# Kernel tuning notes

Measured on AMD Instinct MI355X. Metric: run time of the kernel, lower is better.

Reference implementation:

```python
import jax, jax.numpy as jnp
import numpy as np
import math

B, N, D, H, K = 32, 512, 768, 12, 8  # batch, patches, hidden_dim, heads, n_topic_groups
HD = D // H


def setup_inputs() -> dict:
    key = jax.random.key(0)
    ks = jax.random.split(key, 12)
    hidden_states = jax.random.normal(ks[0], (B, N, D), jnp.float32)
    # group ids in 1..K, every group present (required by original sorted-dict indexing)
    tid = jax.random.permutation(ks[1], (jnp.arange(B, dtype=jnp.int64) % K) + 1)
    s = 1.0 / math.sqrt(D)
    def lin(k):
        kw, kb = jax.random.split(k)
        return (jax.random.normal(kw, (D, D), jnp.float32) * s,
                jax.random.normal(kb, (D,), jnp.float32) * s)
    Wq, bq = lin(ks[2])
    Wk, bk = lin(ks[3])
    Wv, bv = lin(ks[4])
    Wo, bo = lin(ks[5])
    Wc, bc = lin(ks[6])  # Conv1d(D, D, kernel_size=1) == pointwise linear
    return dict(hidden_states=hidden_states, tid=tid, Wq=Wq, bq=bq, Wk=Wk, bk=bk,
                Wv=Wv, bv=bv, Wo=Wo, bo=bo, Wc=Wc, bc=bc)


def reference(hidden_states, tid, Wq, bq, Wk, bk, Wv, bv, Wo, bo, Wc, bc):
    # --- context(): per-group context_aware + mean, scattered back ---
    # context_aware(x) = mean over group of (x + conv1x1(x)); conv is pointwise so
    # it commutes with grouping -> compute per-sample then segment-mean.
    y = hidden_states + jnp.einsum('bnd,ed->bne', hidden_states, Wc) + bc  # [B,N,D]
    seg = tid - 1  # ids are 1..K
    sums = jax.ops.segment_sum(y, seg, num_segments=K)                      # [K,N,D]
    counts = jax.ops.segment_sum(jnp.ones((B,), y.dtype), seg, num_segments=K)
    means = sums / jnp.maximum(counts, 1.0)[:, None, None]
    contexts = means[seg] + hidden_states                                   # [B,N,D]

    # --- dual-stage attention (dropout rate 0 / eval mode) ---
    def heads(x):  # [B,N,D] -> [B,H,N,HD]
        return x.reshape(B, N, H, HD).transpose(0, 2, 1, 3)

    q = heads(hidden_states @ Wq.T + bq)
    t = heads(contexts @ Wq.T + bq)  # topic_states also passes through self.query
    k = heads(hidden_states @ Wk.T + bk)
    v = heads(hidden_states @ Wv.T + bv)

    scale = 1.0 / math.sqrt(HD)
    p1 = jax.nn.softmax(jnp.einsum('bhqd,bhkd->bhqk', t, k) * scale, axis=-1)
    v_t = jnp.einsum('bhqk,bhkd->bhqd', p1, v)
    p2 = jax.nn.softmax(jnp.einsum('bhqd,bhkd->bhqk', q, t) * scale, axis=-1)
    ctx = jnp.einsum('bhqk,bhkd->bhqd', p2, v_t)

    ctx = ctx.transpose(0, 2, 1, 3).reshape(B, N, D)
    return ctx @ Wo.T + bo
```

## Files before the change

kernel.cpp:

```cpp
#include <hip/hip_runtime.h>
#include <hip/hip_bf16.h>


typedef __bf16 bf16_t;
typedef __bf16 bf16x8 __attribute__((ext_vector_type(8)));
typedef __bf16 bf16x4 __attribute__((ext_vector_type(4)));
typedef float f32x4 __attribute__((ext_vector_type(4)));

#define B_ 32
#define N_ 512
#define D_ 768
#define H_ 12
#define HD_ 64
#define K_ 8
#define ND_ (N_ * D_)

typedef __attribute__((address_space(1))) unsigned int as1_u32;
typedef __attribute__((address_space(3))) unsigned int as3_u32;

__device__ __forceinline__ void glds16(const void* g, void* l) {
  __builtin_amdgcn_global_load_lds((as1_u32*)g, (as3_u32*)l, 16, 0, 0);
}

__device__ __forceinline__ f32x4 mfma16(bf16x8 a, bf16x8 b, f32x4 c) {
  return __builtin_amdgcn_mfma_f32_16x16x32_bf16(a, b, c, 0, 0, 0);
}

__device__ __forceinline__ bf16x8 addv8(bf16x8 a, bf16x8 b) {
  bf16x8 o;
#pragma unroll
  for (int j = 0; j < 8; ++j) o[j] = (bf16_t)((float)a[j] + (float)b[j]);
  return o;
}

__device__ __forceinline__ int seg_of(const int* tid, int b) {
  const bool is64 = (tid[1] == 0);
  int v = is64 ? (int)((const long long*)tid)[b] : tid[b];
  return v - 1;
}

__global__ __launch_bounds__(256) void k_cvt_all(
    const float* __restrict__ x, const float* __restrict__ Wq,
    const float* __restrict__ Wk, const float* __restrict__ Wv,
    const float* __restrict__ Wc, const float* __restrict__ Wo,
    bf16_t* __restrict__ Xb, bf16_t* __restrict__ Wqb,
    bf16_t* __restrict__ Wkb, bf16_t* __restrict__ Wvb,
    bf16_t* __restrict__ Wcb, bf16_t* __restrict__ Wob) {
  int bid = blockIdx.x;
  const float* in;
  bf16_t* out;
  if (bid < 6144) {
    in = x; out = Xb;
  } else {
    const int wi = (bid - 6144) / 288;
    bid = (bid - 6144) % 288;
    in = wi == 0 ? Wq : wi == 1 ? Wk : wi == 2 ? Wv : wi == 3 ? Wc : Wo;
    out = wi == 0 ? Wqb : wi == 1 ? Wkb : wi == 2 ? Wvb : wi == 3 ? Wcb : Wob;
  }
  const size_t i = ((size_t)bid * 256 + threadIdx.x) * 8;
  f32x4 a = *(const f32x4*)(in + i);
  f32x4 b = *(const f32x4*)(in + i + 4);
  bf16x8 o;
#pragma unroll
  for (int j = 0; j < 4; ++j) { o[j] = (bf16_t)a[j]; o[4 + j] = (bf16_t)b[j]; }
  *(bf16x8*)(out + i) = o;
}

__device__ __forceinline__ void gemm_core(const bf16_t* __restrict__ A,
                                          const bf16_t* __restrict__ Bw,
                                          char* smem, f32x4 (&acc)[4][4]) {
  const int t = threadIdx.x;
  const int lane = t & 63, w = t >> 6;
  const int quad = lane >> 4, l15 = lane & 15;
  const int r0 = t >> 2;
  const int c0e = (t & 3) * 8;
  const int wbase = w * 1024;
  const int mRow = (w >> 1) * 64, nCol = (w & 1) * 64;

  const bf16_t* ga0 = A + (size_t)r0 * D_ + c0e;
  const bf16_t* ga1 = A + (size_t)(r0 + 64) * D_ + c0e;
  const bf16_t* gb0 = Bw + (size_t)r0 * D_ + c0e;
  const bf16_t* gb1 = Bw + (size_t)(r0 + 64) * D_ + c0e;

  glds16(ga0, smem + wbase);
  glds16(ga1, smem + 4096 + wbase);
  glds16(gb0, smem + 8192 + wbase);
  glds16(gb1, smem + 12288 + wbase);

  for (int kb = 0; kb < 24; ++kb) {
    __syncthreads();
    char* cur = smem + (kb & 1) * 16384;
    char* nxt = smem + ((kb + 1) & 1) * 16384;
    if (kb < 23) {
      const int ko = (kb + 1) * 32;
      glds16(ga0 + ko, nxt + wbase);
      glds16(ga1 + ko, nxt + 4096 + wbase);
      glds16(gb0 + ko, nxt + 8192 + wbase);
      glds16(gb1 + ko, nxt + 12288 + wbase);
    }
    bf16x8 af[4], bfr[4];
#pragma unroll
    for (int mt = 0; mt < 4; ++mt)
      af[mt] = *(const bf16x8*)(cur + (mRow + mt * 16 + l15) * 64 + quad * 16);
#pragma unroll
    for (int nt = 0; nt < 4; ++nt)
      bfr[nt] = *(const bf16x8*)(cur + 8192 + (nCol + nt * 16 + l15) * 64 +
                                 quad * 16);
#pragma unroll
    for (int mt = 0; mt < 4; ++mt)
#pragma unroll
      for (int nt = 0; nt < 4; ++nt)
        acc[mt][nt] = mfma16(af[mt], bfr[nt], acc[mt][nt]);
  }
}

__device__ __forceinline__ void zero_acc(f32x4 (&acc)[4][4]) {
  const f32x4 z = {0.f, 0.f, 0.f, 0.f};
#pragma unroll
  for (int a = 0; a < 4; ++a)
#pragma unroll
    for (int b = 0; b < 4; ++b) acc[a][b] = z;
}

__global__ __launch_bounds__(256) void k_gemm_qkv(
    const bf16_t* __restrict__ X, const bf16_t* __restrict__ Wq,
    const bf16_t* __restrict__ Wk, const bf16_t* __restrict__ Wv,
    const float* __restrict__ bq, const float* __restrict__ bk,
    const float* __restrict__ bv, bf16_t* __restrict__ Q,
    bf16_t* __restrict__ Kb, bf16_t* __restrict__ V) {
  __shared__ alignas(16) char smem[32768];
  const int bid = blockIdx.x;
  const int xcd = bid & 7, i = bid >> 3;
  const int tile = i % 18, rowblk = (i / 18) * 8 + xcd;
  const int wsel = tile / 6, nb = tile % 6;
  const bf16_t* W = wsel == 0 ? Wq : wsel == 1 ? Wk : Wv;
  const float* bias = wsel == 0 ? bq : wsel == 1 ? bk : bv;
  bf16_t* Out = wsel == 0 ? Q : wsel == 1 ? Kb : V;

  f32x4 acc[4][4];
  zero_acc(acc);
  gemm_core(X + (size_t)rowblk * 128 * D_, W + (size_t)nb * 128 * D_, smem,
            acc);

  const int lane = threadIdx.x & 63, w = threadIdx.x >> 6;
  const int quad = lane >> 4, l15 = lane & 15;
  const int mbase = rowblk * 128 + (w >> 1) * 64;
  const int nbase = nb * 128 + (w & 1) * 64;
#pragma unroll
  for (int nt = 0; nt < 4; ++nt) {
    const int col = nbase + nt * 16 + l15;
    const float bb = bias[col];
#pragma unroll
    for (int mt = 0; mt < 4; ++mt)
#pragma unroll
      for (int r = 0; r < 4; ++r) {
        const int row = mbase + mt * 16 + quad * 4 + r;
        Out[(size_t)row * D_ + col] = (bf16_t)(acc[mt][nt][r] + bb);
      }
  }
}

__global__ __launch_bounds__(256) void k_gemm_plain(
    const bf16_t* __restrict__ A, const bf16_t* __restrict__ W,
    const float* __restrict__ bias, const bf16_t* __restrict__ addA,
    void* __restrict__ Out, int outF32, int swz) {
  __shared__ alignas(16) char smem[32768];
  int mblk, nblk;
  if (swz) {
    const int bid = blockIdx.x;
    const int xcd = bid & 7, i = bid >> 3;
    nblk = i % 6;
    mblk = (i / 6) * 8 + xcd;
  } else {
    mblk = blockIdx.x;
    nblk = blockIdx.y;
  }
  f32x4 acc[4][4];
  zero_acc(acc);
  gemm_core(A + (size_t)mblk * 128 * D_, W + (size_t)nblk * 128 * D_, smem,
            acc);
  const int lane = threadIdx.x & 63, w = threadIdx.x >> 6;
  const int quad = lane >> 4, l15 = lane & 15;
  const int mbase = mblk * 128 + (w >> 1) * 64;
  const int nbase = nblk * 128 + (w & 1) * 64;
#pragma unroll
  for (int nt = 0; nt < 4; ++nt) {
    const int col = nbase + nt * 16 + l15;
    const float bb = bias ? bias[col] : 0.f;
#pragma unroll
    for (int mt = 0; mt < 4; ++mt)
#pragma unroll
      for (int r = 0; r < 4; ++r) {
        const int row = mbase + mt * 16 + quad * 4 + r;
        float v = acc[mt][nt][r] + bb;
        if (addA) v += (float)addA[(size_t)row * D_ + col];
        const size_t oi = (size_t)row * D_ + col;
        if (outF32) ((float*)Out)[oi] = v;
        else ((bf16_t*)Out)[oi] = (bf16_t)v;
      }
  }
}

__global__ __launch_bounds__(256) void k_segmean(const float* __restrict__ X,
                                                 const int* __restrict__ tid,
                                                 bf16_t* __restrict__ M) {
  const size_t i = ((size_t)blockIdx.x * 256 + threadIdx.x) * 8;
  float acc[K_][8];
  float cnt[K_];
#pragma unroll
  for (int k = 0; k < K_; ++k) {
    cnt[k] = 0.f;
#pragma unroll
    for (int j = 0; j < 8; ++j) acc[k][j] = 0.f;
  }
  const bool is64 = (tid[1] == 0);
  for (int b = 0; b < B_; ++b) {
    const int s = (is64 ? (int)((const long long*)tid)[b] : tid[b]) - 1;
    const float* p = X + (size_t)b * ND_ + i;
    f32x4 y0 = *(const f32x4*)p;
    f32x4 y1 = *(const f32x4*)(p + 4);
#pragma unroll
    for (int k = 0; k < K_; ++k) {
      const float msk = (s == k) ? 1.f : 0.f;
      cnt[k] += msk;
#pragma unroll
      for (int j = 0; j < 4; ++j) {
        acc[k][j] += msk * y0[j];
        acc[k][4 + j] += msk * y1[j];
      }
    }
  }
#pragma unroll
  for (int k = 0; k < K_; ++k) {
    const float inv = 1.f / fmaxf(cnt[k], 1.f);
    bf16x8 o;
#pragma unroll
    for (int j = 0; j < 8; ++j) o[j] = (bf16_t)(acc[k][j] * inv);
    *(bf16x8*)(M + (size_t)k * ND_ + i) = o;
  }
}

__global__ __launch_bounds__(256) void k_attn(const bf16_t* __restrict__ Qp,
                                              const bf16_t* __restrict__ Kp,
                                              const bf16_t* __restrict__ Vp,
                                              const bf16_t* __restrict__ Madd,
                                              const int* __restrict__ tid,
                                              bf16_t* __restrict__ Op,
                                              int addq) {
  __shared__ alignas(16) __bf16 Kt[64][72];
  __shared__ alignas(16) __bf16 Vt[64][72];
  __shared__ alignas(16) __bf16 Pl[4][32][72];

  const int lane = threadIdx.x & 63, w = threadIdx.x >> 6;
  const int quad = lane >> 4, l15 = lane & 15;
  const int b = blockIdx.y / H_, h = blockIdx.y % H_;
  const int q0 = blockIdx.x * 128 + w * 32;
  const size_t base = (size_t)b * ND_ + h * HD_;
  const float C = 0.18033688011112042f;
  const int sg = seg_of(tid, b);
  const bf16_t* Mh = Madd + (size_t)sg * ND_ + h * HD_;

  bf16x8 aq[2][2];
#pragma unroll
  for (int mt = 0; mt < 2; ++mt)
#pragma unroll
    for (int ks = 0; ks < 2; ++ks) {
      const size_t off = (size_t)(q0 + mt * 16 + l15) * D_ + ks * 32 + quad * 8;
      bf16x8 q = *(const bf16x8*)(Qp + base + off);
      if (addq == 1) q = addv8(q, *(const bf16x8*)(Mh + off));
      aq[mt][ks] = q;
    }

  f32x4 O[2][4];
  float lacc[2][4];
  {
    const f32x4 z = {0.f, 0.f, 0.f, 0.f};
#pragma unroll
    for (int mt = 0; mt < 2; ++mt)
#pragma unroll
      for (int nt = 0; nt < 4; ++nt) O[mt][nt] = z;
#pragma unroll
    for (int mt = 0; mt < 2; ++mt)
#pragma unroll
      for (int r = 0; r < 4; ++r) lacc[mt][r] = 0.f;
  }

  const int sr = threadIdx.x >> 2, sc = threadIdx.x & 3;
  const int sig_sr = ((sr & 15) << 2) | (sr >> 4);

  bf16x8 kr[2], vr[2];
#pragma unroll
  for (int half = 0; half < 2; ++half) {
    const int cc = sc + half * 4;
    const size_t off = (size_t)sr * D_ + cc * 8;
    bf16x8 kv = *(const bf16x8*)(Kp + base + off);
    if (addq == 2) kv = addv8(kv, *(const bf16x8*)(Mh + off));
    kr[half] = kv;
    vr[half] = *(const bf16x8*)(Vp + base + off);
  }

  for (int c0 = 0; c0 < N_; c0 += 64) {
    __syncthreads();
#pragma unroll
    for (int half = 0; half < 2; ++half) {
      const int cc = sc + half * 4;
      *(bf16x8*)(&Kt[sr][cc * 8]) = kr[half];
#pragma unroll
      for (int j = 0; j < 8; ++j) Vt[cc * 8 + j][sig_sr] = vr[half][j];
    }
    __syncthreads();

    if (c0 + 64 < N_) {
#pragma unroll
      for (int half = 0; half < 2; ++half) {
        const int cc = sc + half * 4;
        const size_t off = (size_t)(c0 + 64 + sr) * D_ + cc * 8;
        bf16x8 kv = *(const bf16x8*)(Kp + base + off);
        if (addq == 2) kv = addv8(kv, *(const bf16x8*)(Mh + off));
        kr[half] = kv;
        vr[half] = *(const bf16x8*)(Vp + base + off);
      }
    }

    f32x4 S[2][4];
    {
      const f32x4 z = {0.f, 0.f, 0.f, 0.f};
#pragma unroll
      for (int mt = 0; mt < 2; ++mt)
#pragma unroll
        for (int nt = 0; nt < 4; ++nt) S[mt][nt] = z;
    }
#pragma unroll
    for (int ks = 0; ks < 2; ++ks) {
      bf16x8 bk[4];
#pragma unroll
      for (int nt = 0; nt < 4; ++nt)
        bk[nt] = *(const bf16x8*)(&Kt[nt * 16 + l15][ks * 32 + quad * 8]);
#pragma unroll
      for (int mt = 0; mt < 2; ++mt)
#pragma unroll
        for (int nt = 0; nt < 4; ++nt)
          S[mt][nt] = mfma16(aq[mt][ks], bk[nt], S[mt][nt]);
    }

#pragma unroll
    for (int mt = 0; mt < 2; ++mt)
#pragma unroll
      for (int r = 0; r < 4; ++r) {
        bf16x4 pk;
#pragma unroll
        for (int nt = 0; nt < 4; ++nt) {
          const float p = exp2f(S[mt][nt][r] * C);
          lacc[mt][r] += p;
          pk[nt] = (bf16_t)p;
        }
        *(bf16x4*)(&Pl[w][mt * 16 + quad * 4 + r][l15 * 4]) = pk;
      }

#pragma unroll
    for (int ks2 = 0; ks2 < 2; ++ks2) {
      bf16x8 ap[2], bv[4];
#pragma unroll
      for (int mt = 0; mt < 2; ++mt)
        ap[mt] = *(const bf16x8*)(&Pl[w][mt * 16 + l15][ks2 * 32 + quad * 8]);
#pragma unroll
      for (int nt2 = 0; nt2 < 4; ++nt2)
        bv[nt2] = *(const bf16x8*)(&Vt[nt2 * 16 + l15][ks2 * 32 + quad * 8]);
#pragma unroll
      for (int mt = 0; mt < 2; ++mt)
#pragma unroll
        for (int nt2 = 0; nt2 < 4; ++nt2)
          O[mt][nt2] = mfma16(ap[mt], bv[nt2], O[mt][nt2]);
    }
  }

#pragma unroll
  for (int mt = 0; mt < 2; ++mt)
#pragma unroll
    for (int r = 0; r < 4; ++r) {
      float l = lacc[mt][r];
#pragma unroll
      for (int d = 1; d < 16; d <<= 1) l += __shfl_xor(l, d);
      const float inv = 1.f / l;
      const size_t row = base + (size_t)(q0 + mt * 16 + quad * 4 + r) * D_;
#pragma unroll
      for (int nt2 = 0; nt2 < 4; ++nt2)
        Op[row + nt2 * 16 + l15] = (bf16_t)(O[mt][nt2][r] * inv);
    }
}

__global__ __launch_bounds__(256) void k_zero(float* __restrict__ out) {
  const size_t i = ((size_t)blockIdx.x * 256 + threadIdx.x) * 8;
  f32x4 z = {0.f, 0.f, 0.f, 0.f};
  *(f32x4*)(out + i) = z;
  *(f32x4*)(out + i + 4) = z;
}

extern "C" void kernel_launch(void* const* d_in, const int* in_sizes, int n_in,
                              void* d_out, int out_size, void* d_ws,
                              size_t ws_size, hipStream_t stream) {
  const float* x  = (const float*)d_in[0];
  const int*  tid = (const int*)d_in[1];
  const float* Wq = (const float*)d_in[2];
  const float* bq = (const float*)d_in[3];
  const float* Wk = (const float*)d_in[4];
  const float* bk = (const float*)d_in[5];
  const float* Wv = (const float*)d_in[6];
  const float* bv = (const float*)d_in[7];
  const float* Wo = (const float*)d_in[8];
  const float* bo = (const float*)d_in[9];
  const float* Wc = (const float*)d_in[10];
  const float* bc = (const float*)d_in[11];

  const size_t SZ  = (size_t)B_ * ND_ * sizeof(bf16_t);
  const size_t MSZ = (size_t)K_ * ND_ * sizeof(bf16_t);
  const size_t WSZ = (size_t)D_ * D_ * sizeof(bf16_t);
  if (ws_size < 3 * SZ + MSZ + 5 * WSZ) {
    k_zero<<<6144, 256, 0, stream>>>((float*)d_out);
    return;
  }

  char* ws = (char*)d_ws;
  bf16_t* Qb  = (bf16_t*)(ws);
  bf16_t* Kb  = (bf16_t*)(ws + SZ);
  bf16_t* Vb  = (bf16_t*)(ws + 2 * SZ);
  bf16_t* Mq  = (bf16_t*)(ws + 3 * SZ);
  bf16_t* Wqb = (bf16_t*)(ws + 3 * SZ + MSZ);
  bf16_t* Wkb = (bf16_t*)(ws + 3 * SZ + MSZ + WSZ);
  bf16_t* Wvb = (bf16_t*)(ws + 3 * SZ + MSZ + 2 * WSZ);
  bf16_t* Wcb = (bf16_t*)(ws + 3 * SZ + MSZ + 3 * WSZ);
  bf16_t* Wob = (bf16_t*)(ws + 3 * SZ + MSZ + 4 * WSZ);
  bf16_t* Mx = Qb;
  bf16_t* Mb = Kb;
  bf16_t* VT = (bf16_t*)d_out;
  bf16_t* Xb = (bf16_t*)d_out + (size_t)B_ * ND_;
  bf16_t* CTX = Kb;

  k_cvt_all<<<7584, 256, 0, stream>>>(x, Wq, Wk, Wv, Wc, Wo, Xb, Wqb, Wkb,
                                      Wvb, Wcb, Wob);
  k_segmean<<<192, 256, 0, stream>>>(x, tid, Mx);
  k_gemm_plain<<<dim3(32, 6), 256, 0, stream>>>(Mx, Wcb, bc, Mx, Mb, 0, 0);
  k_gemm_plain<<<dim3(32, 6), 256, 0, stream>>>(Mb, Wqb, nullptr, nullptr, Mq,
                                                0, 0);
  k_gemm_qkv<<<2304, 256, 0, stream>>>(Xb, Wqb, Wkb, Wvb, bq, bk, bv, Qb, Kb,
                                       Vb);
  k_attn<<<dim3(4, B_ * H_), 256, 0, stream>>>(Qb, Kb, Vb, Mq, tid, VT, 1);
  k_attn<<<dim3(4, B_ * H_), 256, 0, stream>>>(Qb, Qb, VT, Mq, tid, CTX, 2);
  k_gemm_plain<<<768, 256, 0, stream>>>(CTX, Wob, bo, nullptr, d_out, 1, 1);
}
```

Before: 419.1 us.

## Use 256x256 tiles with 4-stage LDS pipeline for QKV and output GEMMs

Replaces the 128x128 GEMM tiles for the QKV projection and the output projection with 256x256 tiles run by 512-thread workgroups. A new core keeps a 4-deep ring of LDS stages with explicit vmcnt waits, raises wave priority around the MFMA block, and remaps block ids so neighbouring tiles land on the same XCD. The goal is higher arithmetic intensity and better latency hiding on the two large GEMMs. In exchange it uses 128KB of LDS and more accumulator registers per block, and the launch grids become small (576 and 192 blocks), which may leave CUs idle.

```diff
diff --git a/kernel.cpp b/kernel.cpp
--- a/kernel.cpp
+++ b/kernel.cpp
@@ -114,6 +114,66 @@
   }
 }
 
+#define NKT_ 24
+
+__device__ __forceinline__ void gemm_core256(const bf16_t* __restrict__ A,
+                                             const bf16_t* __restrict__ Bw,
+                                             char* smem, f32x4 (&acc)[8][4]) {
+  const int t = threadIdx.x;
+  const int lane = t & 63, w = t >> 6;
+  const int quad = lane >> 4, l15 = lane & 15;
+  const int wr = w >> 2, wc = w & 3;
+  const int ldsW = w * 1024;
+
+  const bf16_t* gA = A + (size_t)(w * 16 + l15) * D_ + quad * 8;
+  const bf16_t* gB = Bw + (size_t)(wr * 64 + wc * 16 + l15) * D_ + quad * 8;
+
+  auto stage = [&](int kt) {
+    char* slot = smem + (kt & 3) * 32768;
+    const int ko = kt * 32;
+    glds16(gA + ko, slot + ldsW);
+    glds16(gA + 128 * D_ + ko, slot + 8192 + ldsW);
+    glds16(gB + ko, slot + 16384 + ldsW);
+    glds16(gB + 128 * D_ + ko, slot + 24576 + ldsW);
+  };
+
+  stage(0); stage(1); stage(2);
+  asm volatile("s_waitcnt vmcnt(8)" ::: "memory");
+  __builtin_amdgcn_s_barrier();
+  asm volatile("" ::: "memory");
+
+  for (int kt = 0; kt < NKT_; ++kt) {
+    if (kt < NKT_ - 3) stage(kt + 3);
+    const char* slot = smem + (kt & 3) * 32768;
+    const char* aBase = slot + wr * 8192 + quad * 256 + l15 * 16;
+    const char* bBase = slot + 16384 + wc * 4096 + quad * 256 + l15 * 16;
+    bf16x8 af[8], bfr[4];
+#pragma unroll
+    for (int mt = 0; mt < 8; ++mt)
+      af[mt] = *(const bf16x8*)(aBase + mt * 1024);
+#pragma unroll
+    for (int nt = 0; nt < 4; ++nt)
+      bfr[nt] = *(const bf16x8*)(bBase + nt * 1024);
+    __builtin_amdgcn_s_setprio(1);
+#pragma unroll
+    for (int mt = 0; mt < 8; ++mt)
+#pragma unroll
+      for (int nt = 0; nt < 4; ++nt)
+        acc[mt][nt] = mfma16(af[mt], bfr[nt], acc[mt][nt]);
+    __builtin_amdgcn_s_setprio(0);
+    if (kt < NKT_ - 1) {
+      if (kt < NKT_ - 3)
+        asm volatile("s_waitcnt vmcnt(8)" ::: "memory");
+      else if (kt == NKT_ - 3)
+        asm volatile("s_waitcnt vmcnt(4)" ::: "memory");
+      else
+        asm volatile("s_waitcnt vmcnt(0)" ::: "memory");
+      __builtin_amdgcn_s_barrier();
+      asm volatile("" ::: "memory");
+    }
+  }
+}
+
 __device__ __forceinline__ void zero_acc(f32x4 (&acc)[4][4]) {
   const f32x4 z = {0.f, 0.f, 0.f, 0.f};
 #pragma unroll
@@ -122,36 +182,42 @@
     for (int b = 0; b < 4; ++b) acc[a][b] = z;
 }
 
-__global__ __launch_bounds__(256) void k_gemm_qkv(
+__global__ __launch_bounds__(512, 2) void k_gemm_qkv256(
     const bf16_t* __restrict__ X, const bf16_t* __restrict__ Wq,
     const bf16_t* __restrict__ Wk, const bf16_t* __restrict__ Wv,
     const float* __restrict__ bq, const float* __restrict__ bk,
     const float* __restrict__ bv, bf16_t* __restrict__ Q,
     bf16_t* __restrict__ Kb, bf16_t* __restrict__ V) {
-  __shared__ alignas(16) char smem[32768];
+  __shared__ alignas(16) char smem[131072];
   const int bid = blockIdx.x;
-  const int xcd = bid & 7, i = bid >> 3;
-  const int tile = i % 18, rowblk = (i / 18) * 8 + xcd;
-  const int wsel = tile / 6, nb = tile % 6;
+  const int wg = (bid & 7) * 72 + (bid >> 3);
+  const int rowblk = wg / 9, tile = wg % 9;
+  const int wsel = tile / 3, nb = tile % 3;
   const bf16_t* W = wsel == 0 ? Wq : wsel == 1 ? Wk : Wv;
   const float* bias = wsel == 0 ? bq : wsel == 1 ? bk : bv;
   bf16_t* Out = wsel == 0 ? Q : wsel == 1 ? Kb : V;
 
-  f32x4 acc[4][4];
-  zero_acc(acc);
-  gemm_core(X + (size_t)rowblk * 128 * D_, W + (size_t)nb * 128 * D_, smem,
-            acc);
+  f32x4 acc[8][4];
+  {
+    const f32x4 z = {0.f, 0.f, 0.f, 0.f};
+#pragma unroll
+    for (int a = 0; a < 8; ++a)
+#pragma unroll
+      for (int b = 0; b < 4; ++b) acc[a][b] = z;
+  }
+  gemm_core256(X + (size_t)rowblk * 256 * D_, W + (size_t)nb * 256 * D_, smem,
+               acc);
 
   const int lane = threadIdx.x & 63, w = threadIdx.x >> 6;
   const int quad = lane >> 4, l15 = lane & 15;
-  const int mbase = rowblk * 128 + (w >> 1) * 64;
-  const int nbase = nb * 128 + (w & 1) * 64;
+  const int mbase = rowblk * 256 + (w >> 2) * 128;
+  const int nbase = nb * 256 + (w & 3) * 64;
 #pragma unroll
   for (int nt = 0; nt < 4; ++nt) {
     const int col = nbase + nt * 16 + l15;
     const float bb = bias[col];
 #pragma unroll
-    for (int mt = 0; mt < 4; ++mt)
+    for (int mt = 0; mt < 8; ++mt)
 #pragma unroll
       for (int r = 0; r < 4; ++r) {
         const int row = mbase + mt * 16 + quad * 4 + r;
@@ -160,21 +226,49 @@
   }
 }
 
+__global__ __launch_bounds__(512, 2) void k_gemm_wo256(
+    const bf16_t* __restrict__ A, const bf16_t* __restrict__ W,
+    const float* __restrict__ bias, float* __restrict__ Out) {
+  __shared__ alignas(16) char smem[131072];
+  const int bid = blockIdx.x;
+  const int wg = (bid & 7) * 24 + (bid >> 3);
+  const int rowblk = wg / 3, nb = wg % 3;
+
+  f32x4 acc[8][4];
+  {
+    const f32x4 z = {0.f, 0.f, 0.f, 0.f};
+#pragma unroll
+    for (int a = 0; a < 8; ++a)
+#pragma unroll
+      for (int b = 0; b < 4; ++b) acc[a][b] = z;
+  }
+  gemm_core256(A + (size_t)rowblk * 256 * D_, W + (size_t)nb * 256 * D_, smem,
+               acc);
+
+  const int lane = threadIdx.x & 63, w = threadIdx.x >> 6;
+  const int quad = lane >> 4, l15 = lane & 15;
+  const int mbase = rowblk * 256 + (w >> 2) * 128;
+  const int nbase = nb * 256 + (w & 3) * 64;
+#pragma unroll
+  for (int nt = 0; nt < 4; ++nt) {
+    const int col = nbase + nt * 16 + l15;
+    const float bb = bias[col];
+#pragma unroll
+    for (int mt = 0; mt < 8; ++mt)
+#pragma unroll
+      for (int r = 0; r < 4; ++r) {
+        const int row = mbase + mt * 16 + quad * 4 + r;
+        Out[(size_t)row * D_ + col] = acc[mt][nt][r] + bb;
+      }
+  }
+}
+
 __global__ __launch_bounds__(256) void k_gemm_plain(
     const bf16_t* __restrict__ A, const bf16_t* __restrict__ W,
     const float* __restrict__ bias, const bf16_t* __restrict__ addA,
-    void* __restrict__ Out, int outF32, int swz) {
+    void* __restrict__ Out, int outF32) {
   __shared__ alignas(16) char smem[32768];
-  int mblk, nblk;
-  if (swz) {
-    const int bid = blockIdx.x;
-    const int xcd = bid & 7, i = bid >> 3;
-    nblk = i % 6;
-    mblk = (i / 6) * 8 + xcd;
-  } else {
-    mblk = blockIdx.x;
-    nblk = blockIdx.y;
-  }
+  const int mblk = blockIdx.x, nblk = blockIdx.y;
   f32x4 acc[4][4];
   zero_acc(acc);
   gemm_core(A + (size_t)mblk * 128 * D_, W + (size_t)nblk * 128 * D_, smem,
@@ -439,12 +533,12 @@
   k_cvt_all<<<7584, 256, 0, stream>>>(x, Wq, Wk, Wv, Wc, Wo, Xb, Wqb, Wkb,
                                       Wvb, Wcb, Wob);
   k_segmean<<<192, 256, 0, stream>>>(x, tid, Mx);
-  k_gemm_plain<<<dim3(32, 6), 256, 0, stream>>>(Mx, Wcb, bc, Mx, Mb, 0, 0);
+  k_gemm_plain<<<dim3(32, 6), 256, 0, stream>>>(Mx, Wcb, bc, Mx, Mb, 0);
   k_gemm_plain<<<dim3(32, 6), 256, 0, stream>>>(Mb, Wqb, nullptr, nullptr, Mq,
-                                                0, 0);
-  k_gemm_qkv<<<2304, 256, 0, stream>>>(Xb, Wqb, Wkb, Wvb, bq, bk, bv, Qb, Kb,
-                                       Vb);
+                                                0);
+  k_gemm_qkv256<<<576, 512, 0, stream>>>(Xb, Wqb, Wkb, Wvb, bq, bk, bv, Qb,
+                                         Kb, Vb);
   k_attn<<<dim3(4, B_ * H_), 256, 0, stream>>>(Qb, Kb, Vb, Mq, tid, VT, 1);
   k_attn<<<dim3(4, B_ * H_), 256, 0, stream>>>(Qb, Qb, VT, Mq, tid, CTX, 2);
-  k_gemm_plain<<<768, 256, 0, stream>>>(CTX, Wob, bo, nullptr, d_out, 1, 1);
-}
+  k_gemm_wo256<<<192, 512, 0, stream>>>(CTX, Wob, bo, (float*)d_out);
+}
```

New measurement: 425.3 us. About the same (+1.5%).

## Triple-buffer GEMM LDS tiles with vmcnt waits and fragment-ordered layout

Applied to the files above, without the earlier changes.

Moves the shared GEMM core from double to triple buffering, prefetching two K-tiles ahead. It replaces __syncthreads with an explicit s_waitcnt vmcnt plus s_barrier so the newest stage can stay in flight. Global-to-LDS loads are remapped so each wave writes a 16x32 tile in MFMA fragment order, making LDS reads contiguous per lane and avoiding bank conflicts. The cost is LDS growing from 32KB to 48KB per block, which may reduce occupancy.

```diff
diff --git a/kernel.cpp b/kernel.cpp
--- a/kernel.cpp
+++ b/kernel.cpp
@@ -72,45 +72,60 @@
   const int t = threadIdx.x;
   const int lane = t & 63, w = t >> 6;
   const int quad = lane >> 4, l15 = lane & 15;
-  const int r0 = t >> 2;
-  const int c0e = (t & 3) * 8;
   const int wbase = w * 1024;
   const int mRow = (w >> 1) * 64, nCol = (w & 1) * 64;
 
-  const bf16_t* ga0 = A + (size_t)r0 * D_ + c0e;
-  const bf16_t* ga1 = A + (size_t)(r0 + 64) * D_ + c0e;
-  const bf16_t* gb0 = Bw + (size_t)r0 * D_ + c0e;
-  const bf16_t* gb1 = Bw + (size_t)(r0 + 64) * D_ + c0e;
-
-  glds16(ga0, smem + wbase);
-  glds16(ga1, smem + 4096 + wbase);
-  glds16(gb0, smem + 8192 + wbase);
-  glds16(gb1, smem + 12288 + wbase);
-
+  const bf16_t* gA = A + (size_t)(w * 16 + l15) * D_ + quad * 8;
+  const bf16_t* gB = Bw + (size_t)(w * 16 + l15) * D_ + quad * 8;
+
+  auto stage = [&](int kt, char* slot) {
+    const int ko = kt * 32;
+    glds16(gA + ko, slot + wbase);
+    glds16(gA + 64 * D_ + ko, slot + 4096 + wbase);
+    glds16(gB + ko, slot + 8192 + wbase);
+    glds16(gB + 64 * D_ + ko, slot + 12288 + wbase);
+  };
+
+  int aoff[4], boff[4];
+#pragma unroll
+  for (int mt = 0; mt < 4; ++mt) {
+    const int r = mRow + mt * 16;
+    aoff[mt] = (r >> 6) * 4096 + ((r >> 4) & 3) * 1024;
+    const int rb = nCol + mt * 16;
+    boff[mt] = 8192 + (rb >> 6) * 4096 + ((rb >> 4) & 3) * 1024;
+  }
+  const int lbyte = quad * 256 + l15 * 16;
+
+  stage(0, smem);
+  stage(1, smem + 16384);
+
+  int cs = 0;
   for (int kb = 0; kb < 24; ++kb) {
-    __syncthreads();
-    char* cur = smem + (kb & 1) * 16384;
-    char* nxt = smem + ((kb + 1) & 1) * 16384;
-    if (kb < 23) {
-      const int ko = (kb + 1) * 32;
-      glds16(ga0 + ko, nxt + wbase);
-      glds16(ga1 + ko, nxt + 4096 + wbase);
-      glds16(gb0 + ko, nxt + 8192 + wbase);
-      glds16(gb1 + ko, nxt + 12288 + wbase);
+    if (kb < 23)
+      asm volatile("s_waitcnt vmcnt(4)" ::: "memory");
+    else
+      asm volatile("s_waitcnt vmcnt(0)" ::: "memory");
+    __builtin_amdgcn_s_barrier();
+    char* cur = smem + cs * 16384;
+    if (kb < 22) {
+      const int ns = cs;
+      char* tgt = smem + ((cs + 2) % 3) * 16384;
+      (void)ns;
+      stage(kb + 2, tgt);
     }
     bf16x8 af[4], bfr[4];
 #pragma unroll
     for (int mt = 0; mt < 4; ++mt)
-      af[mt] = *(const bf16x8*)(cur + (mRow + mt * 16 + l15) * 64 + quad * 16);
+      af[mt] = *(const bf16x8*)(cur + aoff[mt] + lbyte);
 #pragma unroll
     for (int nt = 0; nt < 4; ++nt)
-      bfr[nt] = *(const bf16x8*)(cur + 8192 + (nCol + nt * 16 + l15) * 64 +
-                                 quad * 16);
+      bfr[nt] = *(const bf16x8*)(cur + boff[nt] + lbyte);
 #pragma unroll
     for (int mt = 0; mt < 4; ++mt)
 #pragma unroll
       for (int nt = 0; nt < 4; ++nt)
         acc[mt][nt] = mfma16(af[mt], bfr[nt], acc[mt][nt]);
+    cs = (cs + 1) == 3 ? 0 : cs + 1;
   }
 }
 
@@ -128,7 +143,7 @@
     const float* __restrict__ bq, const float* __restrict__ bk,
     const float* __restrict__ bv, bf16_t* __restrict__ Q,
     bf16_t* __restrict__ Kb, bf16_t* __restrict__ V) {
-  __shared__ alignas(16) char smem[32768];
+  __shared__ alignas(16) char smem[49152];
   const int bid = blockIdx.x;
   const int xcd = bid & 7, i = bid >> 3;
   const int tile = i % 18, rowblk = (i / 18) * 8 + xcd;
@@ -164,7 +179,7 @@
     const bf16_t* __restrict__ A, const bf16_t* __restrict__ W,
     const float* __restrict__ bias, const bf16_t* __restrict__ addA,
     void* __restrict__ Out, int outF32, int swz) {
-  __shared__ alignas(16) char smem[32768];
+  __shared__ alignas(16) char smem[49152];
   int mblk, nblk;
   if (swz) {
     const int bid = blockIdx.x;
```

After: 447.4 us. 6.8% more time.
